# Kernel tuning notes

Hardware: AMD Instinct MI355X
Metric: run time of the kernel (lower is better)

## Reference

```python
import jax, jax.numpy as jnp
import numpy as np

N_NODES = 100000
N_EDGES = 3200000
D_FEAT = 128
HIDDEN = 64
N_GRAPHS = 64


def gcn_conv(x, W, b, src, dst, deg_inv_sqrt):
    # PyG GCNConv: h = D^-1/2 (A+I) D^-1/2 (x @ W) + b, with self-loops.
    h = x @ W  # [N, out]
    coeff = deg_inv_sqrt[src] * deg_inv_sqrt[dst]  # [E]
    agg = jax.ops.segment_sum(coeff[:, None] * h[src], dst, num_segments=N_NODES)
    # self-loop contribution: deg^-1 * h
    agg = agg + (deg_inv_sqrt * deg_inv_sqrt)[:, None] * h
    return agg + b


def setup_inputs() -> dict:
    key = jax.random.key(0)
    ks = jax.random.split(key, 16)
    x = jax.random.normal(ks[0], (N_NODES, D_FEAT), dtype=jnp.float32)
    edge_index = jax.random.randint(ks[1], (2, N_EDGES), 0, N_NODES, dtype=jnp.int64)
    batch = jnp.sort(jax.random.randint(ks[2], (N_NODES,), 0, N_GRAPHS, dtype=jnp.int64))
    sc_in = 1.0 / np.sqrt(D_FEAT)
    sc_h = 1.0 / np.sqrt(HIDDEN)
    return {
        "x": x,
        "edge_index": edge_index,
        "batch": batch,
        "W1": jax.random.uniform(ks[3], (D_FEAT, HIDDEN), jnp.float32, -sc_in, sc_in),
        "b1": jnp.zeros((HIDDEN,), jnp.float32),
        "mlpW": jax.random.uniform(ks[4], (HIDDEN, HIDDEN), jnp.float32, -sc_h, sc_h),
        "mlpb": jax.random.uniform(ks[5], (HIDDEN,), jnp.float32, -sc_h, sc_h),
        "W2": jax.random.uniform(ks[6], (HIDDEN, HIDDEN), jnp.float32, -sc_h, sc_h),
        "b2": jnp.zeros((HIDDEN,), jnp.float32),
        "W3": jax.random.uniform(ks[7], (HIDDEN, HIDDEN), jnp.float32, -sc_h, sc_h),
        "b3": jnp.zeros((HIDDEN,), jnp.float32),
        "linW": jax.random.uniform(ks[8], (HIDDEN, 1), jnp.float32, -sc_h, sc_h),
        "linb": jax.random.uniform(ks[9], (1,), jnp.float32, -sc_h, sc_h),
    }


def reference(x, edge_index, batch, W1, b1, mlpW, mlpb, W2, b2, W3, b3, linW, linb):
    src, dst = edge_index[0], edge_index[1]
    # symmetric gcn_norm degrees (with self-loop), computed once from dst
    deg = jax.ops.segment_sum(jnp.ones((N_EDGES,), x.dtype), dst, num_segments=N_NODES) + 1.0
    deg_inv_sqrt = jax.lax.rsqrt(deg)

    h = jax.nn.relu(gcn_conv(x, W1, b1, src, dst, deg_inv_sqrt))
    h = jax.nn.relu(h @ mlpW + mlpb)  # mlp1 (Linear); edge_index arg in source is a no-op
    h = jax.nn.relu(gcn_conv(h, W2, b2, src, dst, deg_inv_sqrt))
    h = jax.nn.relu(gcn_conv(h, W3, b3, src, dst, deg_inv_sqrt))

    # global_mean_pool over graphs
    sums = jax.ops.segment_sum(h, batch, num_segments=N_GRAPHS)  # [G, H]
    counts = jax.ops.segment_sum(jnp.ones((N_NODES,), h.dtype), batch, num_segments=N_GRAPHS)
    pooled = sums / jnp.maximum(counts, 1.0)[:, None]

    # dropout p=0.5 is identity in eval mode
    return pooled @ linW + linb  # [G, 1]
```

## Files before the change

kernel.cpp:

```cpp
#include <hip/hip_runtime.h>

#define NN 100000
#define NE 3200000
#define DF 128
#define NH 64
#define NG 64

#define BKN 1024
#define NB2 ((NN + BKN - 1) / BKN)
#define CAP2 34000
#define PART_E 8192
#define PART_T 512
#define PART_NBLK ((NE + PART_E - 1) / PART_E)
#define ELLW 64

typedef _Float16 h16;
typedef unsigned char f8;
typedef __fp16 hv2 __attribute__((ext_vector_type(2)));
typedef __fp16 hv4 __attribute__((ext_vector_type(4)));
typedef float fv4 __attribute__((ext_vector_type(4)));

#define FSCALE 16.0f
#define INV_FSCALE 0.0625f

__device__ __forceinline__ f8 to_f8(float v) {
    int pk = __builtin_amdgcn_cvt_pk_fp8_f32(v, v, 0, false);
    return (f8)(pk & 0xFF);
}

__device__ __forceinline__ float dot2h(unsigned a, unsigned b, float c) {
    return __builtin_amdgcn_fdot2(__builtin_bit_cast(hv2, a),
                                  __builtin_bit_cast(hv2, b), c, false);
}

__device__ __forceinline__ unsigned pack_pair(float v) {
    int nb = __builtin_amdgcn_mov_dpp(__builtin_bit_cast(int, v), 0xB1, 0xF, 0xF, true);
    return __builtin_bit_cast(unsigned,
        __builtin_amdgcn_cvt_pkrtz(v, __builtin_bit_cast(float, nb)));
}

__device__ __forceinline__ unsigned pack_rtn(float a, float b) {
    unsigned ua = (unsigned)__builtin_bit_cast(unsigned short, (h16)a);
    unsigned ub = (unsigned)__builtin_bit_cast(unsigned short, (h16)b);
    return ua | (ub << 16);
}


__global__ void k_init(int* __restrict__ bcur) {
    int i = threadIdx.x;
    if (i < NB2) bcur[i] = i * CAP2;
}


__global__ __launch_bounds__(PART_T) void k_part(const int* __restrict__ src,
                                                 const int* __restrict__ dst,
                                                 int* __restrict__ bcur,
                                                 int* __restrict__ tmp) {
    __shared__ int ds[PART_E];
    __shared__ int hist[NB2];
    __shared__ int base[NB2];
    int t = threadIdx.x;
    int e0 = blockIdx.x * PART_E;
    int ne = NE - e0; if (ne > PART_E) ne = PART_E;

    for (int b = t; b < NB2; b += PART_T) hist[b] = 0;
    __syncthreads();
    for (int i = t; i < ne; i += PART_T) {
        int d = dst[e0 + i];
        ds[i] = d;
        atomicAdd(&hist[d >> 10], 1);
    }
    __syncthreads();
    for (int b = t; b < NB2; b += PART_T)
        base[b] = atomicAdd(&bcur[b], hist[b]);
    __syncthreads();
    for (int i = t; i < ne; i += PART_T) {
        int d = ds[i];
        int s = src[e0 + i];
        int pos = atomicAdd(&base[d >> 10], 1);
        tmp[pos] = (s << 10) | (d & (BKN - 1));
    }
}


__global__ __launch_bounds__(1024) void k_build(const int* __restrict__ bcur,
                                                const int* __restrict__ tmp,
                                                float* __restrict__ dis,
                                                int* __restrict__ cnt,
                                                int* __restrict__ csr,
                                                float* __restrict__ sums,
                                                f8* __restrict__ A,
                                                f8* __restrict__ B) {
    __shared__ int h[BKN];
    __shared__ int cur[BKN];
    int b = blockIdx.x, t = threadIdx.x;
    if (b == 0) { for (int i = t; i < NG * NH + NG; i += 1024) sums[i] = 0.f; }
    if (b == 1 && t < NH) {
        A[(size_t)NN * NH + t] = 0;
        B[(size_t)NN * NH + t] = 0;
    }
    h[t] = 0;
    __syncthreads();
    int beg = b * CAP2, end = bcur[b];
    for (int i = beg + t; i < end; i += 1024) atomicAdd(&h[tmp[i] & (BKN - 1)], 1);
    __syncthreads();
    int node = b * BKN + t;
    int real = h[t];
    int rmax = h[t & ~1] > h[t | 1] ? h[t & ~1] : h[t | 1];
    int common = (rmax + 3) & ~3;
    if (node < NN) {
        dis[node] = rsqrtf((float)real + 1.0f);
        cnt[node] = common;
    }
    cur[t] = 0;
    __syncthreads();
    for (int i = beg + t; i < end; i += 1024) {
        int e = tmp[i];
        int d = e & (BKN - 1);
        int j = atomicAdd(&cur[d], 1);
        int nd = b * BKN + d;
        int pos = ((nd >> 1) << 7) + ((j >> 2) << 3) + ((nd & 1) << 2) + (j & 3);
        csr[pos] = (e >> 10) << 6;
    }
    __syncthreads();
    if (node < NN) {
        int pbase = (node >> 1) << 7;
        int half = (node & 1) << 2;
        for (int j = real; j < common; j++)
            csr[pbase + ((j >> 2) << 3) + half + (j & 3)] = NN << 6;
    }
}


__global__ __launch_bounds__(256) void k_gemm1(const float* __restrict__ x,
                                               const float* __restrict__ W1,
                                               const float* __restrict__ dis,
                                               f8* __restrict__ out) {
    int t = threadIdx.x;
    int lane = t & 63;
    int tile = blockIdx.x * 4 + (t >> 6);
    if (tile >= NN / 16) return;
    int r16 = lane & 15, g4 = lane >> 4;

    hv4 b[4][8];
#pragma unroll
    for (int s = 0; s < 8; s++) {
#pragma unroll
        for (int ct = 0; ct < 4; ct++) {
            const float* wp = W1 + (s * 16 + g4 * 4) * NH + ct * 16 + r16;
            hv4 bb;
            bb[0] = (h16)wp[0];
            bb[1] = (h16)wp[NH];
            bb[2] = (h16)wp[2 * NH];
            bb[3] = (h16)wp[3 * NH];
            b[ct][s] = bb;
        }
    }

    int nb = tile * 16;
    const float* xw = x + (size_t)(nb + r16) * DF + g4 * 4;
    fv4 xr[8];
#pragma unroll
    for (int s = 0; s < 8; s++) xr[s] = *(const fv4*)(xw + s * 16);

    fv4 acc[4] = {fv4{0.f, 0.f, 0.f, 0.f}, fv4{0.f, 0.f, 0.f, 0.f},
                  fv4{0.f, 0.f, 0.f, 0.f}, fv4{0.f, 0.f, 0.f, 0.f}};
#pragma unroll
    for (int s = 0; s < 8; s++) {
        hv4 a;
        a[0] = (h16)xr[s][0]; a[1] = (h16)xr[s][1];
        a[2] = (h16)xr[s][2]; a[3] = (h16)xr[s][3];
#pragma unroll
        for (int ct = 0; ct < 4; ct++)
            acc[ct] = __builtin_amdgcn_mfma_f32_16x16x16f16(a, b[ct][s], acc[ct], 0, 0, 0);
    }

    float dv[4];
#pragma unroll
    for (int r = 0; r < 4; r++) dv[r] = dis[nb + g4 * 4 + r] * FSCALE;
#pragma unroll
    for (int ct = 0; ct < 4; ct++) {
#pragma unroll
        for (int r = 0; r < 4; r++) {
            int n = nb + g4 * 4 + r;
            out[((unsigned)n << 6) | (unsigned)(ct * 16 + r16)] = to_f8(dv[r] * acc[ct][r]);
        }
    }
}


__device__ __forceinline__ float f8_ld(const f8* __restrict__ hs, unsigned off) {
    return __builtin_amdgcn_cvt_f32_fp8((int)hs[off], 0);
}

#define ACC8(qa, qb)                                                    \
    do {                                                                \
        a0 += f8_ld(hs, ((unsigned)(qa).x) | lane);                     \
        a1 += f8_ld(hs, ((unsigned)(qa).y) | lane);                     \
        a0 += f8_ld(hs, ((unsigned)(qa).z) | lane);                     \
        a1 += f8_ld(hs, ((unsigned)(qa).w) | lane);                     \
        b0 += f8_ld(hs, ((unsigned)(qb).x) | lane);                     \
        b1 += f8_ld(hs, ((unsigned)(qb).y) | lane);                     \
        b0 += f8_ld(hs, ((unsigned)(qb).z) | lane);                     \
        b1 += f8_ld(hs, ((unsigned)(qb).w) | lane);                     \
    } while (0)

__device__ __forceinline__ void gather_pair(const int* __restrict__ csr,
                                            const int* __restrict__ cnt,
                                            const f8* __restrict__ hs,
                                            int p, unsigned lane,
                                            float& g0, float& g1) {
    int beg = __builtin_amdgcn_readfirstlane(p << 7);
    int len = __builtin_amdgcn_readfirstlane(cnt[2 * p]);
    int end = beg + 2 * len;
    float a0 = f8_ld(hs, ((unsigned)(2 * p) << 6) | lane);
    float b0 = f8_ld(hs, ((unsigned)(2 * p + 1) << 6) | lane);
    float a1 = 0.f, b1 = 0.f;
    int k = beg;
    if (k + 16 <= end) {
        int4 qa = *(const int4*)(csr + k);
        int4 qb = *(const int4*)(csr + k + 4);
        int4 qc = *(const int4*)(csr + k + 8);
        int4 qd = *(const int4*)(csr + k + 12);
        for (; k + 32 <= end; k += 16) {
            int4 na = *(const int4*)(csr + k + 16);
            int4 nb = *(const int4*)(csr + k + 20);
            int4 nc = *(const int4*)(csr + k + 24);
            int4 nd = *(const int4*)(csr + k + 28);
            ACC8(qa, qb);
            ACC8(qc, qd);
            qa = na; qb = nb; qc = nc; qd = nd;
        }
        ACC8(qa, qb);
        ACC8(qc, qd);
        k += 16;
    }
    if (k + 8 <= end) {
        int4 qa = *(const int4*)(csr + k);
        int4 qb = *(const int4*)(csr + k + 4);
        ACC8(qa, qb);
    }
    g0 = a0 + a1;
    g1 = b0 + b1;
}


__global__ __launch_bounds__(1024) void k_gather_mm2(const int* __restrict__ cnt,
                                                     const int* __restrict__ csr,
                                                     const float* __restrict__ dis,
                                                     const f8* __restrict__ hs,
                                                     const float* __restrict__ bin,
                                                     const float* __restrict__ W1m,
                                                     const float* __restrict__ bmid,
                                                     const float* __restrict__ W2m,
                                                     f8* __restrict__ outp) {
    __shared__ unsigned w1p[(NH / 2) * NH];
    __shared__ unsigned w2p[(NH / 2) * NH];
    __shared__ float b_in[NH], b_mid[NH];
    int t = threadIdx.x;
    for (int i = t; i < (NH / 2) * NH; i += 1024) {
        int k2 = i >> 6, o = i & 63;
        w1p[i] = pack_rtn(W1m[(2 * k2) * NH + o], W1m[(2 * k2 + 1) * NH + o]);
        w2p[i] = pack_rtn(W2m[(2 * k2) * NH + o], W2m[(2 * k2 + 1) * NH + o]);
    }
    if (t < NH) { b_in[t] = bin[t]; b_mid[t] = bmid[t]; }
    __syncthreads();

    int wave = t >> 6, lane = t & 63;
    int p = blockIdx.x * 16 + wave;
    int n0 = 2 * p, n1 = 2 * p + 1;
    float d0 = dis[n0], d1 = dis[n1];

    float g0, g1;
    gather_pair(csr, cnt, hs, p, (unsigned)lane, g0, g1);
    float v0 = fmaxf(g0 * (d0 * INV_FSCALE) + b_in[lane], 0.f);
    float v1 = fmaxf(g1 * (d1 * INV_FSCALE) + b_in[lane], 0.f);

    unsigned pv0 = pack_pair(v0), pv1 = pack_pair(v1);
    float m0 = 0.f, m1 = 0.f;
#pragma unroll
    for (int k2 = 0; k2 < 32; k2++) {
        unsigned wv = w1p[k2 * NH + lane];
        m0 = dot2h((unsigned)__builtin_amdgcn_readlane((int)pv0, 2 * k2), wv, m0);
        m1 = dot2h((unsigned)__builtin_amdgcn_readlane((int)pv1, 2 * k2), wv, m1);
    }
    m0 = fmaxf(m0 + b_mid[lane], 0.f);
    m1 = fmaxf(m1 + b_mid[lane], 0.f);

    unsigned pm0 = pack_pair(m0), pm1 = pack_pair(m1);
    float o0 = 0.f, o1 = 0.f;
#pragma unroll
    for (int k2 = 0; k2 < 32; k2++) {
        unsigned wv = w2p[k2 * NH + lane];
        o0 = dot2h((unsigned)__builtin_amdgcn_readlane((int)pm0, 2 * k2), wv, o0);
        o1 = dot2h((unsigned)__builtin_amdgcn_readlane((int)pm1, 2 * k2), wv, o1);
    }
    outp[((unsigned)n0 << 6) | (unsigned)lane] = to_f8(d0 * o0 * FSCALE);
    outp[((unsigned)n1 << 6) | (unsigned)lane] = to_f8(d1 * o1 * FSCALE);
}


__global__ __launch_bounds__(1024) void k_gather_mm1(const int* __restrict__ cnt,
                                                     const int* __restrict__ csr,
                                                     const float* __restrict__ dis,
                                                     const f8* __restrict__ hs,
                                                     const float* __restrict__ bin,
                                                     const float* __restrict__ W1m,
                                                     f8* __restrict__ outp) {
    __shared__ unsigned w1p[(NH / 2) * NH];
    __shared__ float b_in[NH];
    int t = threadIdx.x;
    for (int i = t; i < (NH / 2) * NH; i += 1024) {
        int k2 = i >> 6, o = i & 63;
        w1p[i] = pack_rtn(W1m[(2 * k2) * NH + o], W1m[(2 * k2 + 1) * NH + o]);
    }
    if (t < NH) b_in[t] = bin[t];
    __syncthreads();

    int wave = t >> 6, lane = t & 63;
    int p = blockIdx.x * 16 + wave;
    int n0 = 2 * p, n1 = 2 * p + 1;
    float d0 = dis[n0], d1 = dis[n1];

    float g0, g1;
    gather_pair(csr, cnt, hs, p, (unsigned)lane, g0, g1);
    float v0 = fmaxf(g0 * (d0 * INV_FSCALE) + b_in[lane], 0.f);
    float v1 = fmaxf(g1 * (d1 * INV_FSCALE) + b_in[lane], 0.f);

    unsigned pv0 = pack_pair(v0), pv1 = pack_pair(v1);
    float o0 = 0.f, o1 = 0.f;
#pragma unroll
    for (int k2 = 0; k2 < 32; k2++) {
        unsigned wv = w1p[k2 * NH + lane];
        o0 = dot2h((unsigned)__builtin_amdgcn_readlane((int)pv0, 2 * k2), wv, o0);
        o1 = dot2h((unsigned)__builtin_amdgcn_readlane((int)pv1, 2 * k2), wv, o1);
    }
    outp[((unsigned)n0 << 6) | (unsigned)lane] = to_f8(d0 * o0 * FSCALE);
    outp[((unsigned)n1 << 6) | (unsigned)lane] = to_f8(d1 * o1 * FSCALE);
}


__global__ __launch_bounds__(1024) void k_gather_pool(const int* __restrict__ cnt,
                                                      const int* __restrict__ csr,
                                                      const float* __restrict__ dis,
                                                      const f8* __restrict__ hs,
                                                      const float* __restrict__ b3,
                                                      const int* __restrict__ batch,
                                                      float* __restrict__ sums,
                                                      float* __restrict__ cntf) {
    __shared__ float rows[32][NH];
    __shared__ int gids[32];
    int t = threadIdx.x;
    int wave = t >> 6, lane = t & 63;
    int p = blockIdx.x * 16 + wave;
    int n0 = 2 * p, n1 = 2 * p + 1;
    {
        float d0 = dis[n0], d1 = dis[n1];
        float g0, g1;
        gather_pair(csr, cnt, hs, p, (unsigned)lane, g0, g1);
        rows[2 * wave][lane]     = fmaxf(g0 * (d0 * INV_FSCALE) + b3[lane], 0.f);
        rows[2 * wave + 1][lane] = fmaxf(g1 * (d1 * INV_FSCALE) + b3[lane], 0.f);
        if (lane == 0) { gids[2 * wave] = batch[n0]; gids[2 * wave + 1] = batch[n1]; }
    }
    __syncthreads();
    if (wave == 0) {
        float acc = 0.f; float cl = 0.f;
        int cur = gids[0];
        for (int i = 0; i < 32; i++) {
            int g = gids[i];
            if (g != cur) {
                atomicAdd(&sums[cur * NH + lane], acc);
                if (lane == 0) atomicAdd(&cntf[cur], cl);
                acc = 0.f; cl = 0.f; cur = g;
            }
            acc += rows[i][lane];
            cl += 1.f;
        }
        atomicAdd(&sums[cur * NH + lane], acc);
        if (lane == 0) atomicAdd(&cntf[cur], cl);
    }
}


__global__ void k_final(const float* __restrict__ sums, const float* __restrict__ cnt,
                        const float* __restrict__ linW, const float* __restrict__ linb,
                        float* __restrict__ out) {
    int g = blockIdx.x;
    int lane = threadIdx.x;
    float v = sums[g * NH + lane] * linW[lane];
#pragma unroll
    for (int off = 32; off > 0; off >>= 1) v += __shfl_down(v, off);
    if (lane == 0) out[g] = v / fmaxf(cnt[g], 1.f) + linb[0];
}


extern "C" void kernel_launch(void* const* d_in, const int* in_sizes, int n_in,
                              void* d_out, int out_size, void* d_ws, size_t ws_size,
                              hipStream_t stream) {
    const float* x    = (const float*)d_in[0];
    const int*   ei   = (const int*)d_in[1];
    const int*   batch= (const int*)d_in[2];
    const float* W1   = (const float*)d_in[3];
    const float* b1   = (const float*)d_in[4];
    const float* mlpW = (const float*)d_in[5];
    const float* mlpb = (const float*)d_in[6];
    const float* W2   = (const float*)d_in[7];
    const float* b2   = (const float*)d_in[8];
    const float* W3   = (const float*)d_in[9];
    const float* b3   = (const float*)d_in[10];
    const float* linW = (const float*)d_in[11];
    const float* linb = (const float*)d_in[12];
    float* out = (float*)d_out;

    char* p = (char*)d_ws;
    int*   csr  = (int*)p;                p += (size_t)NN * ELLW * 4;
    f8*    A    = (f8*)p;                 p += (size_t)(NN + 1) * NH;
    f8*    B    = (f8*)p;                 p += (size_t)(NN + 1) * NH;
    int*   tmp  = (int*)p;                p += (size_t)NB2 * CAP2 * 4;
    float* dis  = (float*)p;              p += NN * 4;
    float* sums = (float*)p;              p += NG * NH * 4;
    float* cntf = (float*)p;              p += NG * 4;
    int*   cnt  = (int*)p;                p += NN * 4;
    int*   bcur = (int*)p;                p += 128 * 4;

    const int* src = ei;
    const int* dst = ei + NE;

    k_init<<<1, 128, 0, stream>>>(bcur);
    k_part<<<PART_NBLK, PART_T, 0, stream>>>(src, dst, bcur, tmp);
    k_build<<<NB2, 1024, 0, stream>>>(bcur, tmp, dis, cnt, csr, sums, A, B);

    k_gemm1<<<(NN / 16 + 3) / 4, 256, 0, stream>>>(x, W1, dis, A);
    k_gather_mm2<<<NN / 32, 1024, 0, stream>>>(cnt, csr, dis, A, b1, mlpW, mlpb, W2, B);

    k_gather_mm1<<<NN / 32, 1024, 0, stream>>>(cnt, csr, dis, B, b2, W3, A);

    k_gather_pool<<<NN / 32, 1024, 0, stream>>>(cnt, csr, dis, A, b3, batch, sums, cntf);

    k_final<<<NG, 64, 0, stream>>>(sums, cntf, linW, linb, out);
}
```

Baseline: 369.6 us.

## Gather two fp8 features per lane with half-wave per node and interleaved CSR

Changes the CSR slot layout so the neighbour lists of the two nodes in a pair are interleaved element by element, and reduces the padding granularity from 4 to 2. Each wave now splits into two halves, one per node, and each lane loads two adjacent fp8 features as a 16-bit load converted with a packed fp8-to-f32 instruction. This halves the number of gather load instructions per edge and cuts padding waste. The cost is one divergent select per index and a changed readlane pattern in the follow-up matvec.

```diff
diff --git a/kernel.cpp b/kernel.cpp
--- a/kernel.cpp
+++ b/kernel.cpp
@@ -16,9 +16,11 @@
 
 typedef _Float16 h16;
 typedef unsigned char f8;
+typedef unsigned short u16;
 typedef __fp16 hv2 __attribute__((ext_vector_type(2)));
 typedef __fp16 hv4 __attribute__((ext_vector_type(4)));
 typedef float fv4 __attribute__((ext_vector_type(4)));
+typedef float fv2 __attribute__((ext_vector_type(2)));
 
 #define FSCALE 16.0f
 #define INV_FSCALE 0.0625f
@@ -26,6 +28,10 @@
 __device__ __forceinline__ f8 to_f8(float v) {
     int pk = __builtin_amdgcn_cvt_pk_fp8_f32(v, v, 0, false);
     return (f8)(pk & 0xFF);
+}
+
+__device__ __forceinline__ fv2 cvtpk8(unsigned u) {
+    return __builtin_amdgcn_cvt_pk_f32_fp8((int)u, false);
 }
 
 __device__ __forceinline__ float dot2h(unsigned a, unsigned b, float c) {
@@ -107,7 +113,7 @@
     int node = b * BKN + t;
     int real = h[t];
     int rmax = h[t & ~1] > h[t | 1] ? h[t & ~1] : h[t | 1];
-    int common = (rmax + 3) & ~3;
+    int common = (rmax + 1) & ~1;
     if (node < NN) {
         dis[node] = rsqrtf((float)real + 1.0f);
         cnt[node] = common;
@@ -119,15 +125,15 @@
         int d = e & (BKN - 1);
         int j = atomicAdd(&cur[d], 1);
         int nd = b * BKN + d;
-        int pos = ((nd >> 1) << 7) + ((j >> 2) << 3) + ((nd & 1) << 2) + (j & 3);
+        int pos = ((nd >> 1) << 7) + (j << 1) + (nd & 1);
         csr[pos] = (e >> 10) << 6;
     }
     __syncthreads();
     if (node < NN) {
         int pbase = (node >> 1) << 7;
-        int half = (node & 1) << 2;
+        int half1 = node & 1;
         for (int j = real; j < common; j++)
-            csr[pbase + ((j >> 2) << 3) + half + (j & 3)] = NN << 6;
+            csr[pbase + (j << 1) + half1] = NN << 6;
     }
 }
 
@@ -189,59 +195,45 @@
 }
 
 
-__device__ __forceinline__ float f8_ld(const f8* __restrict__ hs, unsigned off) {
-    return __builtin_amdgcn_cvt_f32_fp8((int)hs[off], 0);
-}
-
-#define ACC8(qa, qb)                                                    \
-    do {                                                                \
-        a0 += f8_ld(hs, ((unsigned)(qa).x) | lane);                     \
-        a1 += f8_ld(hs, ((unsigned)(qa).y) | lane);                     \
-        a0 += f8_ld(hs, ((unsigned)(qa).z) | lane);                     \
-        a1 += f8_ld(hs, ((unsigned)(qa).w) | lane);                     \
-        b0 += f8_ld(hs, ((unsigned)(qb).x) | lane);                     \
-        b1 += f8_ld(hs, ((unsigned)(qb).y) | lane);                     \
-        b0 += f8_ld(hs, ((unsigned)(qb).z) | lane);                     \
-        b1 += f8_ld(hs, ((unsigned)(qb).w) | lane);                     \
-    } while (0)
-
-__device__ __forceinline__ void gather_pair(const int* __restrict__ csr,
-                                            const int* __restrict__ cnt,
-                                            const f8* __restrict__ hs,
-                                            int p, unsigned lane,
-                                            float& g0, float& g1) {
-    int beg = __builtin_amdgcn_readfirstlane(p << 7);
-    int len = __builtin_amdgcn_readfirstlane(cnt[2 * p]);
-    int end = beg + 2 * len;
-    float a0 = f8_ld(hs, ((unsigned)(2 * p) << 6) | lane);
-    float b0 = f8_ld(hs, ((unsigned)(2 * p + 1) << 6) | lane);
-    float a1 = 0.f, b1 = 0.f;
-    int k = beg;
-    if (k + 16 <= end) {
-        int4 qa = *(const int4*)(csr + k);
-        int4 qb = *(const int4*)(csr + k + 4);
-        int4 qc = *(const int4*)(csr + k + 8);
-        int4 qd = *(const int4*)(csr + k + 12);
-        for (; k + 32 <= end; k += 16) {
-            int4 na = *(const int4*)(csr + k + 16);
-            int4 nb = *(const int4*)(csr + k + 20);
-            int4 nc = *(const int4*)(csr + k + 24);
-            int4 nd = *(const int4*)(csr + k + 28);
-            ACC8(qa, qb);
-            ACC8(qc, qd);
-            qa = na; qb = nb; qc = nc; qd = nd;
-        }
-        ACC8(qa, qb);
-        ACC8(qc, qd);
-        k += 16;
-    }
-    if (k + 8 <= end) {
-        int4 qa = *(const int4*)(csr + k);
-        int4 qb = *(const int4*)(csr + k + 4);
-        ACC8(qa, qb);
-    }
-    g0 = a0 + a1;
-    g1 = b0 + b1;
+__device__ __forceinline__ fv2 gather_half(const int* __restrict__ csr,
+                                           const int* __restrict__ cnt,
+                                           const f8* __restrict__ hs,
+                                           int p, int lane) {
+    int half = lane >> 5;
+    unsigned c2 = ((unsigned)(lane & 31)) << 1;
+    int ng2 = __builtin_amdgcn_readfirstlane(cnt[2 * p]) >> 1;
+    const int4* q4 = (const int4*)(csr + (p << 7));
+    const char* hb = (const char*)hs;
+
+    unsigned selfoff = (((unsigned)(2 * p + half)) << 6) | c2;
+    fv2 a0 = cvtpk8(*(const u16*)(hb + selfoff));
+    fv2 a1 = {0.f, 0.f};
+
+    int i = 0;
+    for (; i + 2 <= ng2; i += 2) {
+        int4 ca = q4[i];
+        int4 cb = q4[i + 1];
+        unsigned o0 = (unsigned)(half ? ca.y : ca.x) | c2;
+        unsigned o1 = (unsigned)(half ? ca.w : ca.z) | c2;
+        unsigned o2 = (unsigned)(half ? cb.y : cb.x) | c2;
+        unsigned o3 = (unsigned)(half ? cb.w : cb.z) | c2;
+        unsigned u0 = *(const u16*)(hb + o0);
+        unsigned u1 = *(const u16*)(hb + o1);
+        unsigned u2 = *(const u16*)(hb + o2);
+        unsigned u3 = *(const u16*)(hb + o3);
+        a0 += cvtpk8(u0);
+        a1 += cvtpk8(u1);
+        a0 += cvtpk8(u2);
+        a1 += cvtpk8(u3);
+    }
+    if (i < ng2) {
+        int4 ca = q4[i];
+        unsigned o0 = (unsigned)(half ? ca.y : ca.x) | c2;
+        unsigned o1 = (unsigned)(half ? ca.w : ca.z) | c2;
+        a0 += cvtpk8(*(const u16*)(hb + o0));
+        a1 += cvtpk8(*(const u16*)(hb + o1));
+    }
+    return a0 + a1;
 }
 
 
@@ -271,18 +263,19 @@
     int n0 = 2 * p, n1 = 2 * p + 1;
     float d0 = dis[n0], d1 = dis[n1];
 
-    float g0, g1;
-    gather_pair(csr, cnt, hs, p, (unsigned)lane, g0, g1);
-    float v0 = fmaxf(g0 * (d0 * INV_FSCALE) + b_in[lane], 0.f);
-    float v1 = fmaxf(g1 * (d1 * INV_FSCALE) + b_in[lane], 0.f);
-
-    unsigned pv0 = pack_pair(v0), pv1 = pack_pair(v1);
+    fv2 g = gather_half(csr, cnt, hs, p, lane);
+    float dd = (lane < 32 ? d0 : d1) * INV_FSCALE;
+    fv2 bl = *(const fv2*)&b_in[(lane & 31) * 2];
+    float vx = fmaxf(g.x * dd + bl.x, 0.f);
+    float vy = fmaxf(g.y * dd + bl.y, 0.f);
+    unsigned pv = __builtin_bit_cast(unsigned, __builtin_amdgcn_cvt_pkrtz(vx, vy));
+
     float m0 = 0.f, m1 = 0.f;
 #pragma unroll
     for (int k2 = 0; k2 < 32; k2++) {
         unsigned wv = w1p[k2 * NH + lane];
-        m0 = dot2h((unsigned)__builtin_amdgcn_readlane((int)pv0, 2 * k2), wv, m0);
-        m1 = dot2h((unsigned)__builtin_amdgcn_readlane((int)pv1, 2 * k2), wv, m1);
+        m0 = dot2h((unsigned)__builtin_amdgcn_readlane((int)pv, k2), wv, m0);
+        m1 = dot2h((unsigned)__builtin_amdgcn_readlane((int)pv, 32 + k2), wv, m1);
     }
     m0 = fmaxf(m0 + b_mid[lane], 0.f);
     m1 = fmaxf(m1 + b_mid[lane], 0.f);
@@ -322,18 +315,19 @@
     int n0 = 2 * p, n1 = 2 * p + 1;
     float d0 = dis[n0], d1 = dis[n1];
 
-    float g0, g1;
-    gather_pair(csr, cnt, hs, p, (unsigned)lane, g0, g1);
-    float v0 = fmaxf(g0 * (d0 * INV_FSCALE) + b_in[lane], 0.f);
-    float v1 = fmaxf(g1 * (d1 * INV_FSCALE) + b_in[lane], 0.f);
-
-    unsigned pv0 = pack_pair(v0), pv1 = pack_pair(v1);
+    fv2 g = gather_half(csr, cnt, hs, p, lane);
+    float dd = (lane < 32 ? d0 : d1) * INV_FSCALE;
+    fv2 bl = *(const fv2*)&b_in[(lane & 31) * 2];
+    float vx = fmaxf(g.x * dd + bl.x, 0.f);
+    float vy = fmaxf(g.y * dd + bl.y, 0.f);
+    unsigned pv = __builtin_bit_cast(unsigned, __builtin_amdgcn_cvt_pkrtz(vx, vy));
+
     float o0 = 0.f, o1 = 0.f;
 #pragma unroll
     for (int k2 = 0; k2 < 32; k2++) {
         unsigned wv = w1p[k2 * NH + lane];
-        o0 = dot2h((unsigned)__builtin_amdgcn_readlane((int)pv0, 2 * k2), wv, o0);
-        o1 = dot2h((unsigned)__builtin_amdgcn_readlane((int)pv1, 2 * k2), wv, o1);
+        o0 = dot2h((unsigned)__builtin_amdgcn_readlane((int)pv, k2), wv, o0);
+        o1 = dot2h((unsigned)__builtin_amdgcn_readlane((int)pv, 32 + k2), wv, o1);
     }
     outp[((unsigned)n0 << 6) | (unsigned)lane] = to_f8(d0 * o0 * FSCALE);
     outp[((unsigned)n1 << 6) | (unsigned)lane] = to_f8(d1 * o1 * FSCALE);
@@ -356,10 +350,14 @@
     int n0 = 2 * p, n1 = 2 * p + 1;
     {
         float d0 = dis[n0], d1 = dis[n1];
-        float g0, g1;
-        gather_pair(csr, cnt, hs, p, (unsigned)lane, g0, g1);
-        rows[2 * wave][lane]     = fmaxf(g0 * (d0 * INV_FSCALE) + b3[lane], 0.f);
-        rows[2 * wave + 1][lane] = fmaxf(g1 * (d1 * INV_FSCALE) + b3[lane], 0.f);
+        fv2 g = gather_half(csr, cnt, hs, p, lane);
+        float dd = (lane < 32 ? d0 : d1) * INV_FSCALE;
+        fv2 bl = *(const fv2*)&b3[(lane & 31) * 2];
+        fv2 r;
+        r.x = fmaxf(g.x * dd + bl.x, 0.f);
+        r.y = fmaxf(g.y * dd + bl.y, 0.f);
+        int half = lane >> 5;
+        *(fv2*)&rows[2 * wave + half][(lane & 31) * 2] = r;
         if (lane == 0) { gids[2 * wave] = batch[n0]; gids[2 * wave + 1] = batch[n1]; }
     }
     __syncthreads();
```

Measured after the change: 426.2 us. 1.15x slower.
